# Kernel tuning notes

Measured on AMD Instinct MI355X. Metric: run time of the kernel, lower is better.

The kernel has to match this reference:

```python
import jax, jax.numpy as jnp
import numpy as np


def _structure_constants():
    # Octonion multiplication table: e_i * e_j = sum_k C[i,j,k] e_k.
    # e0 is the real unit; imaginary triples follow the standard Fano-plane
    # convention (Baez): e_a e_b = e_c for the cyclic triples below.
    C = np.zeros((8, 8, 8), dtype=np.float32)
    C[0, 0, 0] = 1.0
    for i in range(1, 8):
        C[0, i, i] = 1.0   # 1 * e_i = e_i
        C[i, 0, i] = 1.0   # e_i * 1 = e_i
        C[i, i, 0] = -1.0  # e_i * e_i = -1
    triples = [(1, 2, 3), (1, 4, 5), (1, 7, 6), (2, 4, 6), (2, 5, 7), (3, 4, 7), (3, 6, 5)]
    for (a, b, c) in triples:
        for (p, q, r) in ((a, b, c), (b, c, a), (c, a, b)):
            C[p, q, r] = 1.0
            C[q, p, r] = -1.0
    return C


_C = _structure_constants()

IN_FEATURES = 64
OUT_FEATURES = 64
BATCH = (16, 4096)


def setup_inputs() -> dict:
    key = jax.random.key(0)
    kx, kw, kb = jax.random.split(key, 3)
    x = jax.random.normal(kx, (*BATCH, IN_FEATURES, 8), dtype=jnp.float32)
    # 8 octonion-component weight matrices, stacked: [8, out, in]
    scale = 1.0 / np.sqrt(IN_FEATURES * 8)
    W = jax.random.normal(kw, (8, OUT_FEATURES, IN_FEATURES), dtype=jnp.float32) * scale
    b = jax.random.normal(kb, (OUT_FEATURES, 8), dtype=jnp.float32) * 0.01
    return {"x": x, "W": W, "b": b}


def reference(x, W, b):
    # out[..., o, k] = sum_{i,j,f} C[i,j,k] * W[i,o,f] * x[..., f, j] + b[o, k]
    # Fold the sparse structure constants into one block weight, then a single
    # contraction (the fused-GEMM formulation of the original 64-linear loop).
    C = jnp.asarray(_C, dtype=x.dtype)
    Wbig = jnp.einsum('iof,ijk->okfj', W, C)        # [out, 8, in, 8]
    out = jnp.einsum('...fj,okfj->...ok', x, Wbig)  # [..., out, 8]
    return out + b
```

## Files before the change

kernel.cpp:

```cpp
#include <hip/hip_runtime.h>
#include <hip/hip_bf16.h>

typedef __attribute__((ext_vector_type(8))) short short8;
typedef __attribute__((ext_vector_type(4))) float f32x4;

#define BM 256
#define BN 256
#define BK 64
#define LDST 72
#define NKT 8
#define TILE_ELEMS (256 * LDST)

static __device__ __forceinline__ unsigned short f2bf(float f) {
    union { __hip_bfloat16 h; unsigned short u; } cv;
    cv.h = __float2bfloat16(f);
    return cv.u;
}

__global__ __launch_bounds__(256) void build_wbig(const float* __restrict__ W,
                                                  unsigned short* __restrict__ Wbig) {
    __shared__ float C[8][8][8];
    const int t = threadIdx.x;
    for (int i = t; i < 512; i += 256) ((float*)C)[i] = 0.0f;
    __syncthreads();
    if (t == 0) {
        C[0][0][0] = 1.0f;
        for (int i = 1; i < 8; ++i) { C[0][i][i] = 1.0f; C[i][0][i] = 1.0f; C[i][i][0] = -1.0f; }
        const int tr[7][3] = {{1,2,3},{1,4,5},{1,7,6},{2,4,6},{2,5,7},{3,4,7},{3,6,5}};
        for (int q = 0; q < 7; ++q) {
            const int a = tr[q][0], b = tr[q][1], c = tr[q][2];
            const int p[3][3] = {{a,b,c},{b,c,a},{c,a,b}};
            for (int u = 0; u < 3; ++u) {
                C[p[u][0]][p[u][1]][p[u][2]] = 1.0f;
                C[p[u][1]][p[u][0]][p[u][2]] = -1.0f;
            }
        }
    }
    __syncthreads();
    const int e = blockIdx.x * 256 + t;
    const int m = e >> 9, kk = e & 511;
    const int o = m >> 3, k = m & 7, f = kk >> 3, j = kk & 7;
    float s = 0.0f;
#pragma unroll
    for (int i = 0; i < 8; ++i) s += C[i][j][k] * W[i * 4096 + o * 64 + f];
    Wbig[e] = f2bf(s);
}

__global__ __launch_bounds__(512, 2) void oct_gemm(const float* __restrict__ X,
                                                   const unsigned short* __restrict__ Wbig,
                                                   const float* __restrict__ Bias,
                                                   float* __restrict__ Out) {
    extern __shared__ unsigned short smem[];
    unsigned short* As[2] = { smem,                  smem + TILE_ELEMS };
    unsigned short* Bs[2] = { smem + 2 * TILE_ELEMS, smem + 3 * TILE_ELEMS };

    const int bid   = blockIdx.x;
    const int xcd   = bid & 7;
    const int ix    = bid >> 3;
    const int mtile = xcd * 32 + (ix >> 1);
    const int ntile = ix & 1;
    const int rowBase = mtile * BM;
    const int colBase = ntile * BN;

    const int t    = threadIdx.x;
    const int lane = t & 63;
    const int wave = t >> 6;
    const int wr   = wave >> 2;
    const int wc   = wave & 3;
    const int l15  = lane & 15;
    const int l4   = lane >> 4;

    const int srow = t >> 3;
    const int scol = (t & 7) * 8;

    const float*          Xrow = X    + (size_t)(rowBase + srow) * 512 + scol;
    const unsigned short* Brow = Wbig + (size_t)(colBase + srow) * 512 + scol;

    f32x4  va[8];
    short8 vb[4];

#define ISSUE_AB(KT) do { _Pragma("unroll") \
    for (int l = 0; l < 4; ++l) { \
        const float* src = Xrow + (size_t)(l * 64) * 512 + (KT); \
        va[2*l]   = *reinterpret_cast<const f32x4*>(src); \
        va[2*l+1] = *reinterpret_cast<const f32x4*>(src + 4); \
    } \
    _Pragma("unroll") \
    for (int l = 0; l < 4; ++l) \
        vb[l] = *reinterpret_cast<const short8*>(Brow + (size_t)(l * 64) * 512 + (KT)); \
    } while (0)

#define WRITE_AB(BUF) do { _Pragma("unroll") \
    for (int l = 0; l < 4; ++l) { \
        short8 p; \
        p[0]=(short)f2bf(va[2*l][0]);   p[1]=(short)f2bf(va[2*l][1]); \
        p[2]=(short)f2bf(va[2*l][2]);   p[3]=(short)f2bf(va[2*l][3]); \
        p[4]=(short)f2bf(va[2*l+1][0]); p[5]=(short)f2bf(va[2*l+1][1]); \
        p[6]=(short)f2bf(va[2*l+1][2]); p[7]=(short)f2bf(va[2*l+1][3]); \
        *reinterpret_cast<short8*>(&As[BUF][(l*64 + srow) * LDST + scol]) = p; \
    } \
    _Pragma("unroll") \
    for (int l = 0; l < 4; ++l) \
        *reinterpret_cast<short8*>(&Bs[BUF][(l*64 + srow) * LDST + scol]) = vb[l]; \
    } while (0)

    f32x4 acc[8][4];
#pragma unroll
    for (int ni = 0; ni < 4; ++ni) {
        const float bv = Bias[colBase + wc * 64 + ni * 16 + l15];
#pragma unroll
        for (int mi = 0; mi < 8; ++mi) acc[mi][ni] = (f32x4){bv, bv, bv, bv};
    }

    ISSUE_AB(0);
    WRITE_AB(0);
    asm volatile("s_waitcnt lgkmcnt(0)" ::: "memory");
    __builtin_amdgcn_s_barrier();

#pragma unroll
    for (int kt = 0; kt < NKT; ++kt) {
        if (kt + 1 < NKT) ISSUE_AB((kt + 1) * BK);
        __builtin_amdgcn_sched_barrier(0);

#pragma unroll
        for (int kk = 0; kk < 2; ++kk) {
            const int kb = kk * 32 + l4 * 8;
            short8 b[4];
#pragma unroll
            for (int ni = 0; ni < 4; ++ni)
                b[ni] = *reinterpret_cast<const short8*>(
                    &Bs[kt & 1][(wc * 64 + ni * 16 + l15) * LDST + kb]);
            __builtin_amdgcn_s_setprio(1);
#pragma unroll
            for (int mi = 0; mi < 8; ++mi) {
                const short8 a = *reinterpret_cast<const short8*>(
                    &As[kt & 1][(wr * 128 + mi * 16 + l15) * LDST + kb]);
#pragma unroll
                for (int ni = 0; ni < 4; ++ni)
                    acc[mi][ni] = __builtin_amdgcn_mfma_f32_16x16x32_bf16(
                        a, b[ni], acc[mi][ni], 0, 0, 0);
            }
            __builtin_amdgcn_s_setprio(0);
        }
        __builtin_amdgcn_sched_barrier(0);

        if (kt + 1 < NKT) WRITE_AB((kt + 1) & 1);

        asm volatile("s_waitcnt lgkmcnt(0)" ::: "memory");
        __builtin_amdgcn_s_barrier();
    }

#pragma unroll
    for (int mi = 0; mi < 8; ++mi) {
        const int row0 = rowBase + wr * 128 + mi * 16 + l4 * 4;
#pragma unroll
        for (int ni = 0; ni < 4; ++ni) {
            const int col = colBase + wc * 64 + ni * 16 + l15;
#pragma unroll
            for (int r = 0; r < 4; ++r)
                Out[(size_t)(row0 + r) * 512 + col] = acc[mi][ni][r];
        }
    }
#undef ISSUE_AB
#undef WRITE_AB
}

extern "C" void kernel_launch(void* const* d_in, const int* in_sizes, int n_in,
                              void* d_out, int out_size, void* d_ws, size_t ws_size,
                              hipStream_t stream) {
    const float* x = (const float*)d_in[0];
    const float* W = (const float*)d_in[1];
    const float* b = (const float*)d_in[2];
    float* out = (float*)d_out;
    unsigned short* Wbig = (unsigned short*)d_ws;

    static bool attr_done = false;
    if (!attr_done) {
        hipFuncSetAttribute((const void*)oct_gemm,
                            hipFuncAttributeMaxDynamicSharedMemorySize,
                            4 * TILE_ELEMS * (int)sizeof(unsigned short));
        attr_done = true;
    }

    build_wbig<<<1024, 256, 0, stream>>>(W, Wbig);
    oct_gemm<<<512, 512, 4 * TILE_ELEMS * sizeof(unsigned short), stream>>>(x, Wbig, b, out);
}
```

Before: 67.06 us.

## Shrink GEMM tiles to 128x256x32 and prefetch global loads two stages ahead

Halves the M tile and the K step, which shrinks LDS use to static shared memory and allows four workgroups per CU under the new launch bounds. Global loads are now issued two K-steps ahead using two register sets, so more memory latency is hidden. The grid doubles to 1024 blocks. In exchange there are twice as many barriers per block, less reuse of each B tile, and an LDS row stride of 36 that may cause bank conflicts.

```diff
diff --git a/kernel.cpp b/kernel.cpp
--- a/kernel.cpp
+++ b/kernel.cpp
@@ -4,12 +4,11 @@
 typedef __attribute__((ext_vector_type(8))) short short8;
 typedef __attribute__((ext_vector_type(4))) float f32x4;
 
-#define BM 256
+#define BM 128
 #define BN 256
-#define BK 64
-#define LDST 72
-#define NKT 8
-#define TILE_ELEMS (256 * LDST)
+#define BK 32
+#define LDST 36
+#define NKT 16
 
 static __device__ __forceinline__ unsigned short f2bf(float f) {
     union { __hip_bfloat16 h; unsigned short u; } cv;
@@ -46,18 +45,17 @@
     Wbig[e] = f2bf(s);
 }
 
-__global__ __launch_bounds__(512, 2) void oct_gemm(const float* __restrict__ X,
+__global__ __launch_bounds__(512, 4) void oct_gemm(const float* __restrict__ X,
                                                    const unsigned short* __restrict__ Wbig,
                                                    const float* __restrict__ Bias,
                                                    float* __restrict__ Out) {
-    extern __shared__ unsigned short smem[];
-    unsigned short* As[2] = { smem,                  smem + TILE_ELEMS };
-    unsigned short* Bs[2] = { smem + 2 * TILE_ELEMS, smem + 3 * TILE_ELEMS };
+    __shared__ unsigned short As[2][BM * LDST];
+    __shared__ unsigned short Bs[2][BN * LDST];
 
     const int bid   = blockIdx.x;
     const int xcd   = bid & 7;
     const int ix    = bid >> 3;
-    const int mtile = xcd * 32 + (ix >> 1);
+    const int mtile = xcd * 64 + (ix >> 1);
     const int ntile = ix & 1;
     const int rowBase = mtile * BM;
     const int colBase = ntile * BN;
@@ -70,61 +68,54 @@
     const int l15  = lane & 15;
     const int l4   = lane >> 4;
 
-    const int srow = t >> 3;
-    const int scol = (t & 7) * 8;
+    const int arow = t >> 2, ac = (t & 3) * 8;
+    const int brow = t >> 1, bc = (t & 1) * 16;
 
-    const float*          Xrow = X    + (size_t)(rowBase + srow) * 512 + scol;
-    const unsigned short* Brow = Wbig + (size_t)(colBase + srow) * 512 + scol;
+    const float*          Xp = X    + (size_t)(rowBase + arow) * 512 + ac;
+    const unsigned short* Bp = Wbig + (size_t)(colBase + brow) * 512 + bc;
 
-    f32x4  va[8];
-    short8 vb[4];
+    f32x4  va[2][2];
+    short8 vb[2][2];
 
-#define ISSUE_AB(KT) do { _Pragma("unroll") \
-    for (int l = 0; l < 4; ++l) { \
-        const float* src = Xrow + (size_t)(l * 64) * 512 + (KT); \
-        va[2*l]   = *reinterpret_cast<const f32x4*>(src); \
-        va[2*l+1] = *reinterpret_cast<const f32x4*>(src + 4); \
-    } \
-    _Pragma("unroll") \
-    for (int l = 0; l < 4; ++l) \
-        vb[l] = *reinterpret_cast<const short8*>(Brow + (size_t)(l * 64) * 512 + (KT)); \
+#define ISSUE(SET, KT) do { \
+    va[SET][0] = *reinterpret_cast<const f32x4*>(Xp + (KT)); \
+    va[SET][1] = *reinterpret_cast<const f32x4*>(Xp + (KT) + 4); \
+    vb[SET][0] = *reinterpret_cast<const short8*>(Bp + (KT)); \
+    vb[SET][1] = *reinterpret_cast<const short8*>(Bp + (KT) + 8); \
     } while (0)
 
-#define WRITE_AB(BUF) do { _Pragma("unroll") \
-    for (int l = 0; l < 4; ++l) { \
-        short8 p; \
-        p[0]=(short)f2bf(va[2*l][0]);   p[1]=(short)f2bf(va[2*l][1]); \
-        p[2]=(short)f2bf(va[2*l][2]);   p[3]=(short)f2bf(va[2*l][3]); \
-        p[4]=(short)f2bf(va[2*l+1][0]); p[5]=(short)f2bf(va[2*l+1][1]); \
-        p[6]=(short)f2bf(va[2*l+1][2]); p[7]=(short)f2bf(va[2*l+1][3]); \
-        *reinterpret_cast<short8*>(&As[BUF][(l*64 + srow) * LDST + scol]) = p; \
-    } \
-    _Pragma("unroll") \
-    for (int l = 0; l < 4; ++l) \
-        *reinterpret_cast<short8*>(&Bs[BUF][(l*64 + srow) * LDST + scol]) = vb[l]; \
+#define WRITE(SET, BUF) do { \
+    short8 p; \
+    p[0]=(short)f2bf(va[SET][0][0]); p[1]=(short)f2bf(va[SET][0][1]); \
+    p[2]=(short)f2bf(va[SET][0][2]); p[3]=(short)f2bf(va[SET][0][3]); \
+    p[4]=(short)f2bf(va[SET][1][0]); p[5]=(short)f2bf(va[SET][1][1]); \
+    p[6]=(short)f2bf(va[SET][1][2]); p[7]=(short)f2bf(va[SET][1][3]); \
+    *reinterpret_cast<short8*>(&As[BUF][arow * LDST + ac]) = p; \
+    *reinterpret_cast<short8*>(&Bs[BUF][brow * LDST + bc]) = vb[SET][0]; \
+    *reinterpret_cast<short8*>(&Bs[BUF][brow * LDST + bc + 8]) = vb[SET][1]; \
     } while (0)
 
-    f32x4 acc[8][4];
+    f32x4 acc[4][4];
 #pragma unroll
     for (int ni = 0; ni < 4; ++ni) {
         const float bv = Bias[colBase + wc * 64 + ni * 16 + l15];
 #pragma unroll
-        for (int mi = 0; mi < 8; ++mi) acc[mi][ni] = (f32x4){bv, bv, bv, bv};
+        for (int mi = 0; mi < 4; ++mi) acc[mi][ni] = (f32x4){bv, bv, bv, bv};
     }
 
-    ISSUE_AB(0);
-    WRITE_AB(0);
+    ISSUE(0, 0);
+    ISSUE(1, BK);
+    WRITE(0, 0);
     asm volatile("s_waitcnt lgkmcnt(0)" ::: "memory");
     __builtin_amdgcn_s_barrier();
 
 #pragma unroll
     for (int kt = 0; kt < NKT; ++kt) {
-        if (kt + 1 < NKT) ISSUE_AB((kt + 1) * BK);
+        if (kt + 2 < NKT) ISSUE(kt & 1, (kt + 2) * BK);
         __builtin_amdgcn_sched_barrier(0);
 
-#pragma unroll
-        for (int kk = 0; kk < 2; ++kk) {
-            const int kb = kk * 32 + l4 * 8;
+        {
+            const int kb = l4 * 8;
             short8 b[4];
 #pragma unroll
             for (int ni = 0; ni < 4; ++ni)
@@ -132,9 +123,9 @@
                     &Bs[kt & 1][(wc * 64 + ni * 16 + l15) * LDST + kb]);
             __builtin_amdgcn_s_setprio(1);
 #pragma unroll
-            for (int mi = 0; mi < 8; ++mi) {
+            for (int mi = 0; mi < 4; ++mi) {
                 const short8 a = *reinterpret_cast<const short8*>(
-                    &As[kt & 1][(wr * 128 + mi * 16 + l15) * LDST + kb]);
+                    &As[kt & 1][(wr * 64 + mi * 16 + l15) * LDST + kb]);
 #pragma unroll
                 for (int ni = 0; ni < 4; ++ni)
                     acc[mi][ni] = __builtin_amdgcn_mfma_f32_16x16x32_bf16(
@@ -144,15 +135,15 @@
         }
         __builtin_amdgcn_sched_barrier(0);
 
-        if (kt + 1 < NKT) WRITE_AB((kt + 1) & 1);
+        if (kt + 1 < NKT) WRITE((kt + 1) & 1, (kt + 1) & 1);
 
         asm volatile("s_waitcnt lgkmcnt(0)" ::: "memory");
         __builtin_amdgcn_s_barrier();
     }
 
 #pragma unroll
-    for (int mi = 0; mi < 8; ++mi) {
-        const int row0 = rowBase + wr * 128 + mi * 16 + l4 * 4;
+    for (int mi = 0; mi < 4; ++mi) {
+        const int row0 = rowBase + wr * 64 + mi * 16 + l4 * 4;
 #pragma unroll
         for (int ni = 0; ni < 4; ++ni) {
             const int col = colBase + wc * 64 + ni * 16 + l15;
@@ -161,8 +152,8 @@
                 Out[(size_t)(row0 + r) * 512 + col] = acc[mi][ni][r];
         }
     }
-#undef ISSUE_AB
-#undef WRITE_AB
+#undef ISSUE
+#undef WRITE
 }
 
 extern "C" void kernel_launch(void* const* d_in, const int* in_sizes, int n_in,
@@ -174,14 +165,6 @@
     float* out = (float*)d_out;
     unsigned short* Wbig = (unsigned short*)d_ws;
 
-    static bool attr_done = false;
-    if (!attr_done) {
-        hipFuncSetAttribute((const void*)oct_gemm,
-                            hipFuncAttributeMaxDynamicSharedMemorySize,
-                            4 * TILE_ELEMS * (int)sizeof(unsigned short));
-        attr_done = true;
-    }
-
     build_wbig<<<1024, 256, 0, stream>>>(W, Wbig);
-    oct_gemm<<<512, 512, 4 * TILE_ELEMS * sizeof(unsigned short), stream>>>(x, Wbig, b, out);
+    oct_gemm<<<1024, 512, 0, stream>>>(x, Wbig, b, out);
 }
```

Result: slower. 174.1 us (+159.6%).

## Stream B tiles via global_load_lds with pre-swizzled layout and deeper A prefetch

Applied to the files above, without the earlier changes.

build_wbig now writes the block weight in a tiled, XOR-swizzled layout so the GEMM can copy B straight from global memory into LDS with global_load_lds, bypassing registers. LDS padding is dropped for B and the swizzle is undone on read to avoid bank conflicts. X loads are prefetched two k-steps ahead using two register buffers, with vmcnt waits tuned to the pipeline depth. This aims to cut the VGPR pressure and LDS store instructions on the B path and hide global latency better, at the cost of more registers held for A and tricky wait-count correctness.

```diff
diff --git a/kernel.cpp b/kernel.cpp
--- a/kernel.cpp
+++ b/kernel.cpp
@@ -3,13 +3,17 @@
 
 typedef __attribute__((ext_vector_type(8))) short short8;
 typedef __attribute__((ext_vector_type(4))) float f32x4;
+typedef __attribute__((address_space(1))) const unsigned int as1_u32;
+typedef __attribute__((address_space(3))) unsigned int as3_u32;
 
 #define BM 256
 #define BN 256
 #define BK 64
-#define LDST 72
+#define LDSTA 72
 #define NKT 8
-#define TILE_ELEMS (256 * LDST)
+#define A_ELE (256 * LDSTA)
+#define B_ELE (256 * 64)
+#define LDS_BYTES ((2 * A_ELE + 2 * B_ELE) * 2)
 
 static __device__ __forceinline__ unsigned short f2bf(float f) {
     union { __hip_bfloat16 h; unsigned short u; } cv;
@@ -17,8 +21,12 @@
     return cv.u;
 }
 
+__device__ __forceinline__ void gload16(const unsigned short* g, unsigned short* l) {
+    __builtin_amdgcn_global_load_lds((as1_u32*)g, (as3_u32*)l, 16, 0, 0);
+}
+
 __global__ __launch_bounds__(256) void build_wbig(const float* __restrict__ W,
-                                                  unsigned short* __restrict__ Wbig) {
+                                                  unsigned short* __restrict__ WbigS) {
     __shared__ float C[8][8][8];
     const int t = threadIdx.x;
     for (int i = t; i < 512; i += 256) ((float*)C)[i] = 0.0f;
@@ -43,16 +51,20 @@
     float s = 0.0f;
 #pragma unroll
     for (int i = 0; i < 8; ++i) s += C[i][j][k] * W[i * 4096 + o * 64 + f];
-    Wbig[e] = f2bf(s);
+
+    const int ntile = m >> 8, row = m & 255;
+    const int kt = kk >> 6, c = kk & 63;
+    const int g_st = (c >> 3) ^ (row & 7);
+    WbigS[((((size_t)(ntile * 8 + kt) * 256 + row) * 8 + g_st) * 8) + (c & 7)] = f2bf(s);
 }
 
 __global__ __launch_bounds__(512, 2) void oct_gemm(const float* __restrict__ X,
-                                                   const unsigned short* __restrict__ Wbig,
+                                                   const unsigned short* __restrict__ WbigS,
                                                    const float* __restrict__ Bias,
                                                    float* __restrict__ Out) {
     extern __shared__ unsigned short smem[];
-    unsigned short* As[2] = { smem,                  smem + TILE_ELEMS };
-    unsigned short* Bs[2] = { smem + 2 * TILE_ELEMS, smem + 3 * TILE_ELEMS };
+    unsigned short* As[2] = { smem,             smem + A_ELE };
+    unsigned short* Bs[2] = { smem + 2 * A_ELE, smem + 2 * A_ELE + B_ELE };
 
     const int bid   = blockIdx.x;
     const int xcd   = bid & 7;
@@ -64,44 +76,39 @@
 
     const int t    = threadIdx.x;
     const int lane = t & 63;
-    const int wave = t >> 6;
-    const int wr   = wave >> 2;
-    const int wc   = wave & 3;
+    const int w    = t >> 6;
+    const int wr   = w >> 2;
+    const int wc   = w & 3;
     const int l15  = lane & 15;
     const int l4   = lane >> 4;
 
     const int srow = t >> 3;
     const int scol = (t & 7) * 8;
-
-    const float*          Xrow = X    + (size_t)(rowBase + srow) * 512 + scol;
-    const unsigned short* Brow = Wbig + (size_t)(colBase + srow) * 512 + scol;
-
-    f32x4  va[8];
-    short8 vb[4];
-
-#define ISSUE_AB(KT) do { _Pragma("unroll") \
+    const float* Xrow = X + (size_t)(rowBase + srow) * 512 + scol;
+
+    f32x4 va0[8], va1[8];
+
+#define ISSUE_A(VA, KT) do { _Pragma("unroll") \
     for (int l = 0; l < 4; ++l) { \
-        const float* src = Xrow + (size_t)(l * 64) * 512 + (KT); \
-        va[2*l]   = *reinterpret_cast<const f32x4*>(src); \
-        va[2*l+1] = *reinterpret_cast<const f32x4*>(src + 4); \
-    } \
-    _Pragma("unroll") \
-    for (int l = 0; l < 4; ++l) \
-        vb[l] = *reinterpret_cast<const short8*>(Brow + (size_t)(l * 64) * 512 + (KT)); \
-    } while (0)
-
-#define WRITE_AB(BUF) do { _Pragma("unroll") \
+        const float* src = Xrow + (size_t)(l * 64) * 512 + (KT) * BK; \
+        VA[2*l]   = *reinterpret_cast<const f32x4*>(src); \
+        VA[2*l+1] = *reinterpret_cast<const f32x4*>(src + 4); \
+    } } while (0)
+
+#define WRITE_A(VA, BUF) do { _Pragma("unroll") \
     for (int l = 0; l < 4; ++l) { \
         short8 p; \
-        p[0]=(short)f2bf(va[2*l][0]);   p[1]=(short)f2bf(va[2*l][1]); \
-        p[2]=(short)f2bf(va[2*l][2]);   p[3]=(short)f2bf(va[2*l][3]); \
-        p[4]=(short)f2bf(va[2*l+1][0]); p[5]=(short)f2bf(va[2*l+1][1]); \
-        p[6]=(short)f2bf(va[2*l+1][2]); p[7]=(short)f2bf(va[2*l+1][3]); \
-        *reinterpret_cast<short8*>(&As[BUF][(l*64 + srow) * LDST + scol]) = p; \
-    } \
-    _Pragma("unroll") \
-    for (int l = 0; l < 4; ++l) \
-        *reinterpret_cast<short8*>(&Bs[BUF][(l*64 + srow) * LDST + scol]) = vb[l]; \
+        p[0]=(short)f2bf(VA[2*l][0]);   p[1]=(short)f2bf(VA[2*l][1]); \
+        p[2]=(short)f2bf(VA[2*l][2]);   p[3]=(short)f2bf(VA[2*l][3]); \
+        p[4]=(short)f2bf(VA[2*l+1][0]); p[5]=(short)f2bf(VA[2*l+1][1]); \
+        p[6]=(short)f2bf(VA[2*l+1][2]); p[7]=(short)f2bf(VA[2*l+1][3]); \
+        *reinterpret_cast<short8*>(&As[BUF][(l*64 + srow) * LDSTA + scol]) = p; \
+    } } while (0)
+
+#define GLOAD_B(BUF, KT) do { _Pragma("unroll") \
+    for (int j = 0; j < 4; ++j) \
+        gload16(WbigS + ((size_t)(ntile * 8 + (KT)) << 14) + (((w * 4 + j) * 64 + lane) << 3), \
+                Bs[BUF] + ((w * 4 + j) << 9)); \
     } while (0)
 
     f32x4 acc[8][4];
@@ -112,29 +119,33 @@
         for (int mi = 0; mi < 8; ++mi) acc[mi][ni] = (f32x4){bv, bv, bv, bv};
     }
 
-    ISSUE_AB(0);
-    WRITE_AB(0);
-    asm volatile("s_waitcnt lgkmcnt(0)" ::: "memory");
+    ISSUE_A(va0, 0);
+    GLOAD_B(0, 0);
+    ISSUE_A(va1, 1);
+    WRITE_A(va0, 0);
+    asm volatile("s_waitcnt vmcnt(8) lgkmcnt(0)" ::: "memory");
     __builtin_amdgcn_s_barrier();
 
 #pragma unroll
     for (int kt = 0; kt < NKT; ++kt) {
-        if (kt + 1 < NKT) ISSUE_AB((kt + 1) * BK);
+        if (kt + 1 < NKT) GLOAD_B((kt + 1) & 1, kt + 1);
+        if (kt + 2 < NKT) { if ((kt & 1) == 0) ISSUE_A(va0, kt + 2); else ISSUE_A(va1, kt + 2); }
         __builtin_amdgcn_sched_barrier(0);
 
 #pragma unroll
         for (int kk = 0; kk < 2; ++kk) {
-            const int kb = kk * 32 + l4 * 8;
             short8 b[4];
 #pragma unroll
-            for (int ni = 0; ni < 4; ++ni)
-                b[ni] = *reinterpret_cast<const short8*>(
-                    &Bs[kt & 1][(wc * 64 + ni * 16 + l15) * LDST + kb]);
+            for (int ni = 0; ni < 4; ++ni) {
+                const int row = wc * 64 + ni * 16 + l15;
+                const int gs  = ((kk * 4 + l4) ^ (l15 & 7)) * 8;
+                b[ni] = *reinterpret_cast<const short8*>(&Bs[kt & 1][row * 64 + gs]);
+            }
             __builtin_amdgcn_s_setprio(1);
 #pragma unroll
             for (int mi = 0; mi < 8; ++mi) {
                 const short8 a = *reinterpret_cast<const short8*>(
-                    &As[kt & 1][(wr * 128 + mi * 16 + l15) * LDST + kb]);
+                    &As[kt & 1][(wr * 128 + mi * 16 + l15) * LDSTA + kk * 32 + l4 * 8]);
 #pragma unroll
                 for (int ni = 0; ni < 4; ++ni)
                     acc[mi][ni] = __builtin_amdgcn_mfma_f32_16x16x32_bf16(
@@ -144,9 +155,14 @@
         }
         __builtin_amdgcn_sched_barrier(0);
 
-        if (kt + 1 < NKT) WRITE_AB((kt + 1) & 1);
-
-        asm volatile("s_waitcnt lgkmcnt(0)" ::: "memory");
+        if (kt + 1 < NKT) { if ((kt & 1) == 0) WRITE_A(va1, 1); else WRITE_A(va0, 0); }
+
+        if (kt + 2 < NKT)
+            asm volatile("s_waitcnt vmcnt(8) lgkmcnt(0)" ::: "memory");
+        else if (kt + 1 < NKT)
+            asm volatile("s_waitcnt vmcnt(0) lgkmcnt(0)" ::: "memory");
+        else
+            asm volatile("s_waitcnt lgkmcnt(0)" ::: "memory");
         __builtin_amdgcn_s_barrier();
     }
 
@@ -161,8 +177,9 @@
                 Out[(size_t)(row0 + r) * 512 + col] = acc[mi][ni][r];
         }
     }
-#undef ISSUE_AB
-#undef WRITE_AB
+#undef ISSUE_A
+#undef WRITE_A
+#undef GLOAD_B
 }
 
 extern "C" void kernel_launch(void* const* d_in, const int* in_sizes, int n_in,
@@ -172,16 +189,15 @@
     const float* W = (const float*)d_in[1];
     const float* b = (const float*)d_in[2];
     float* out = (float*)d_out;
-    unsigned short* Wbig = (unsigned short*)d_ws;
+    unsigned short* WbigS = (unsigned short*)d_ws;
 
     static bool attr_done = false;
     if (!attr_done) {
         hipFuncSetAttribute((const void*)oct_gemm,
-                            hipFuncAttributeMaxDynamicSharedMemorySize,
-                            4 * TILE_ELEMS * (int)sizeof(unsigned short));
+                            hipFuncAttributeMaxDynamicSharedMemorySize, LDS_BYTES);
         attr_done = true;
     }
 
-    build_wbig<<<1024, 256, 0, stream>>>(W, Wbig);
-    oct_gemm<<<512, 512, 4 * TILE_ELEMS * sizeof(unsigned short), stream>>>(x, Wbig, b, out);
-}
+    build_wbig<<<1024, 256, 0, stream>>>(W, WbigS);
+    oct_gemm<<<512, 512, LDS_BYTES, stream>>>(x, WbigS, b, out);
+}
```

After: 65.00 us. -3.1%, faster.
